# Kernel tuning notes

Hardware: AMD Instinct MI355X
Metric: run time of the kernel (lower is better)

The kernel has to match this reference:

```python
import math
import jax, jax.numpy as jnp
import numpy as np

D_MODEL = 1024
HEADS = 16
DH = D_MODEL // HEADS
MAX_REL = 128
LN_EPS = 1e-5


def setup_inputs() -> dict:
    key = jax.random.key(0)
    ks = jax.random.split(key, 6)
    B, T = 4, 2048
    scale = 1.0 / math.sqrt(D_MODEL)
    x = jax.random.normal(ks[0], (B, T, D_MODEL), dtype=jnp.float32)
    Wq = jax.random.normal(ks[1], (D_MODEL, D_MODEL), dtype=jnp.float32) * scale
    Wk = jax.random.normal(ks[2], (D_MODEL, D_MODEL), dtype=jnp.float32) * scale
    Wv = jax.random.normal(ks[3], (D_MODEL, D_MODEL), dtype=jnp.float32) * scale
    Wo = jax.random.normal(ks[4], (D_MODEL, D_MODEL), dtype=jnp.float32) * scale
    # rel bias init as in torch: per-head linspace(0, -2, max_rel+1)
    rel = jnp.tile(jnp.linspace(0.0, -2.0, MAX_REL + 1, dtype=jnp.float32)[None, :], (HEADS, 1))
    ln_gamma = jnp.ones((D_MODEL,), dtype=jnp.float32)
    ln_beta = jnp.zeros((D_MODEL,), dtype=jnp.float32)
    return {"x": x, "Wq": Wq, "Wk": Wk, "Wv": Wv, "Wo": Wo,
            "rel": rel, "ln_gamma": ln_gamma, "ln_beta": ln_beta}


def _layernorm(x, gamma, beta):
    mu = jnp.mean(x, axis=-1, keepdims=True)
    var = jnp.mean(jnp.square(x - mu), axis=-1, keepdims=True)
    return (x - mu) * jax.lax.rsqrt(var + LN_EPS) * gamma + beta


def reference(x, Wq, Wk, Wv, Wo, rel, ln_gamma, ln_beta):
    B, T, D = x.shape
    x0 = x
    xn = _layernorm(x, ln_gamma, ln_beta)
    # projections -> [B, H, T, dh]  (torch Linear: x @ W.T; weights here stored as [out,in])
    def proj(W):
        return (xn @ W.T).reshape(B, T, HEADS, DH).transpose(0, 2, 1, 3)
    q = proj(Wq) / math.sqrt(DH)
    k = proj(Wk)
    v = proj(Wv)
    scores = jnp.einsum('bhid,bhjd->bhij', q, k)  # [B,H,T,T]
    # latency-aware relative bias: bias[h,i,j] = rel[h, min(max(i-j,0), max_rel)]
    i = jnp.arange(T)
    dist = jnp.clip(i[:, None] - i[None, :], 0, MAX_REL)  # [T,T]
    bias = rel[:, dist]  # [H,T,T]
    scores = scores + bias[None]
    causal = i[:, None] >= i[None, :]  # j <= i allowed
    scores = jnp.where(causal[None, None], scores, -jnp.inf)
    attn = jax.nn.softmax(scores, axis=-1)
    y = jnp.einsum('bhij,bhjd->bhid', attn, v)  # [B,H,T,dh]
    y = y.transpose(0, 2, 1, 3).reshape(B, T, D)
    y = y @ Wo.T
    return x0 + y
```

## Files before the change

### kernel.cpp

```cpp
#include <hip/hip_runtime.h>
#include <math.h>

#define TSEQ 2048
#define BATCH 4
#define NH 16
#define DH 64
#define DM 1024
#define NREL 129
#define NEGBIG (-1.0e30f)
#define FIXMAX 8.0f

typedef unsigned short u16;
typedef unsigned int u32;
typedef __attribute__((ext_vector_type(8))) short bf16x8;
typedef __attribute__((ext_vector_type(4))) float f32x4;
typedef __attribute__((ext_vector_type(4))) unsigned short u16x4;

typedef __attribute__((address_space(3))) void lds_void;
typedef const __attribute__((address_space(1))) void g_void;

__device__ inline u16 f2b(float f) {
    union { float f; u32 i; } c; c.f = f;
    u32 x = c.i;
    return (u16)((x + 0x7fffu + ((x >> 16) & 1u)) >> 16);
}

__global__ __launch_bounds__(256) void fill_kernel(float* __restrict__ out, int n, float v) {
    for (int i = blockIdx.x * 256 + threadIdx.x; i < n; i += gridDim.x * 256)
        out[i] = v;
}

__global__ __launch_bounds__(256) void ln_kernel(const float* __restrict__ x,
        const float* __restrict__ gamma, const float* __restrict__ beta,
        u16* __restrict__ xn) {
    const int row = blockIdx.x;
    const int tid = threadIdx.x;
    const float* xr = x + (size_t)row * DM;
    f32x4 xv = *(const f32x4*)(xr + tid * 4);
    float s = xv.x + xv.y + xv.z + xv.w;
    float s2 = xv.x*xv.x + xv.y*xv.y + xv.z*xv.z + xv.w*xv.w;
#pragma unroll
    for (int off = 32; off > 0; off >>= 1) {
        s  += __shfl_down(s, off, 64);
        s2 += __shfl_down(s2, off, 64);
    }
    __shared__ alignas(16) float red[8];
    const int wv = tid >> 6, ln = tid & 63;
    if (ln == 0) { red[wv] = s; red[4 + wv] = s2; }
    __syncthreads();
    s  = red[0] + red[1] + red[2] + red[3];
    s2 = red[4] + red[5] + red[6] + red[7];
    const float mu = s * (1.0f / DM);
    float var = s2 * (1.0f / DM) - mu * mu;
    var = var > 0.0f ? var : 0.0f;
    const float rstd = rsqrtf(var + 1e-5f);
    f32x4 gv = *(const f32x4*)(gamma + tid * 4);
    f32x4 bv = *(const f32x4*)(beta + tid * 4);
    u16x4 ov;
    ov.x = f2b((xv.x - mu) * rstd * gv.x + bv.x);
    ov.y = f2b((xv.y - mu) * rstd * gv.y + bv.y);
    ov.z = f2b((xv.z - mu) * rstd * gv.z + bv.z);
    ov.w = f2b((xv.w - mu) * rstd * gv.w + bv.w);
    *(u16x4*)(xn + (size_t)row * DM + tid * 4) = ov;
}

__global__ __launch_bounds__(256) void cvt3_kernel(const float* __restrict__ a,
        const float* __restrict__ b, const float* __restrict__ c,
        u16* __restrict__ dst) {
    const int i = blockIdx.x * 256 + threadIdx.x;
    const int m = i >> 18;
    const int j = i & 0x3FFFF;
    const float* src = m == 0 ? a : (m == 1 ? b : c);
    const float scale = m == 0 ? 0.125f : 1.0f;
    f32x4 v = *(const f32x4*)(src + (size_t)j * 4);
    u16x4 o;
    o.x = f2b(v.x * scale); o.y = f2b(v.y * scale);
    o.z = f2b(v.z * scale); o.w = f2b(v.w * scale);
    *(u16x4*)(dst + (size_t)i * 4) = o;
}

__global__ __launch_bounds__(256) void cvt1_kernel(const float* __restrict__ src,
        u16* __restrict__ dst, int n4) {
    const int i = blockIdx.x * 256 + threadIdx.x;
    if (i >= n4) return;
    f32x4 v = *(const f32x4*)(src + (size_t)i * 4);
    u16x4 o;
    o.x = f2b(v.x); o.y = f2b(v.y); o.z = f2b(v.z); o.w = f2b(v.w);
    *(u16x4*)(dst + (size_t)i * 4) = o;
}

#define BM 128
#define BN 128
#define BK 32

__global__ __launch_bounds__(256) void gemm_qkv(const u16* __restrict__ A,
        const u16* __restrict__ W3, u16* __restrict__ Qb, u16* __restrict__ Kb,
        u16* __restrict__ Vb) {
    __shared__ alignas(16) u16 sh[8192];
    u16* As = sh;
    u16* Bs = sh + 4096;
    const int id = blockIdx.x + 64 * blockIdx.y;
    const int xcd = id & 7;
    const int k = id >> 3;
    const int xv = xcd * 8 + (k & 7);
    const int yv = k >> 3;
    const int m0 = xv * BM;
    const int mat = yv >> 3;
    const int n0 = (yv & 7) * BN;
    const u16* Wb = W3 + (size_t)mat * DM * DM;
    const int tid = threadIdx.x;
    const int w = tid >> 6;
    const int lane = tid & 63;
    const int quad = lane >> 4, l16 = lane & 15;
    const int wr = (w >> 1) * 64;
    const int wc = (w & 1) * 64;

    const int c0 = w * 2;
    const int srow = c0 * 16 + (lane >> 2);
    const int scol = (lane & 3) * 8;
    const u16* ag = A  + (size_t)(m0 + srow) * DM + scol;
    const u16* bg = Wb + (size_t)(n0 + srow) * DM + scol;
    u16* as0 = As + c0 * 512;
    u16* bs0 = Bs + c0 * 512;

    f32x4 acc[4][4];
#pragma unroll
    for (int i = 0; i < 4; i++)
#pragma unroll
        for (int j = 0; j < 4; j++) acc[i][j] = (f32x4){0.f, 0.f, 0.f, 0.f};

    for (int k0 = 0; k0 < DM; k0 += BK) {
        __builtin_amdgcn_global_load_lds((g_void*)(ag + k0),            (lds_void*)as0,         16, 0, 0);
        __builtin_amdgcn_global_load_lds((g_void*)(ag + k0 + 16 * DM),  (lds_void*)(as0 + 512), 16, 0, 0);
        __builtin_amdgcn_global_load_lds((g_void*)(bg + k0),            (lds_void*)bs0,         16, 0, 0);
        __builtin_amdgcn_global_load_lds((g_void*)(bg + k0 + 16 * DM),  (lds_void*)(bs0 + 512), 16, 0, 0);
        __syncthreads();
        bf16x8 af[4], bfr[4];
#pragma unroll
        for (int mt = 0; mt < 4; mt++)
            af[mt] = *(const bf16x8*)(As + (wr + mt * 16 + l16) * BK + quad * 8);
#pragma unroll
        for (int nt = 0; nt < 4; nt++)
            bfr[nt] = *(const bf16x8*)(Bs + (wc + nt * 16 + l16) * BK + quad * 8);
#pragma unroll
        for (int mt = 0; mt < 4; mt++)
#pragma unroll
            for (int nt = 0; nt < 4; nt++)
                acc[mt][nt] = __builtin_amdgcn_mfma_f32_16x16x32_bf16(af[mt], bfr[nt], acc[mt][nt], 0, 0, 0);
        __syncthreads();
    }

    u16* outb = mat == 0 ? Qb : (mat == 1 ? Kb : Vb);
    const size_t bh = (size_t)(m0 >> 11) * NH + ((n0 + wc) >> 6);
    const int tq = (m0 & 2047) + wr;
    u16* stage = sh + w * 2048;

#pragma unroll
    for (int p = 0; p < 2; p++) {
#pragma unroll
        for (int mt = 0; mt < 4; mt++) {
#pragma unroll
            for (int ntl = 0; ntl < 2; ntl++) {
                const int nt = p * 2 + ntl;
#pragma unroll
                for (int r = 0; r < 4; r++) {
                    const u16 val = f2b(acc[mt][nt][r]);
                    int a;
                    if (mat == 0) {
                        a = mt * 512
                          + ((ntl * 2 + (l16 >> 3)) * 16 + quad * 4 + r) * 8 + (l16 & 7);
                    } else if (mat == 1) {
                        a = ((mt >> 1) * 2 + (quad & 1)) * 512
                          + ((ntl * 2 + (l16 >> 3)) * 16 + (quad >> 1) * 4 + (mt & 1) * 8 + r) * 8
                          + (l16 & 7);
                    } else {
                        a = ((mt >> 1) * 2 + ntl) * 512
                          + (((mt * 2 + (quad >> 1)) & 3) * 16 + l16) * 8
                          + (quad & 1) * 4 + r;
                    }
                    stage[a] = val;
                }
            }
        }
#pragma unroll
        for (int c = 0; c < 4; c++) {
            const bf16x8 vv = *(const bf16x8*)(stage + c * 512 + lane * 8);
            size_t gc;
            if (mat == 0)      gc = (bh * 128 + (tq >> 4) + c) * 2 + p;
            else if (mat == 1) gc = (bh * 64 + (tq >> 5) + (c >> 1)) * 4 + (c & 1) * 2 + p;
            else               gc = (bh * 64 + (tq >> 5) + (c >> 1)) * 4 + p * 2 + (c & 1);
            *(bf16x8*)(outb + gc * 512 + lane * 8) = vv;
        }
    }
}

__global__ __launch_bounds__(256) void gemm_wo(const u16* __restrict__ A,
        const u16* __restrict__ Wb, const float* __restrict__ X0,
        float* __restrict__ out) {
    __shared__ alignas(16) u16 As[BM * BK];
    __shared__ alignas(16) u16 Bs[BN * BK];
    const int id = blockIdx.x + 64 * blockIdx.y;
    const int xcd = id & 7;
    const int k = id >> 3;
    const int m0 = (xcd * 8 + (k & 7)) * BM;
    const int n0 = (k >> 3) * BN;
    const int tid = threadIdx.x;
    const int w = tid >> 6;
    const int lane = tid & 63;
    const int quad = lane >> 4, l16 = lane & 15;
    const int wr = (w >> 1) * 64;
    const int wc = (w & 1) * 64;

    const int c0 = w * 2;
    const int srow = c0 * 16 + (lane >> 2);
    const int scol = (lane & 3) * 8;
    const u16* ag = A  + (size_t)(m0 + srow) * DM + scol;
    const u16* bg = Wb + (size_t)(n0 + srow) * DM + scol;
    u16* as0 = As + c0 * 512;
    u16* bs0 = Bs + c0 * 512;

    f32x4 acc[4][4];
#pragma unroll
    for (int i = 0; i < 4; i++)
#pragma unroll
        for (int j = 0; j < 4; j++) acc[i][j] = (f32x4){0.f, 0.f, 0.f, 0.f};

    for (int k0 = 0; k0 < DM; k0 += BK) {
        __builtin_amdgcn_global_load_lds((g_void*)(ag + k0),            (lds_void*)as0,         16, 0, 0);
        __builtin_amdgcn_global_load_lds((g_void*)(ag + k0 + 16 * DM),  (lds_void*)(as0 + 512), 16, 0, 0);
        __builtin_amdgcn_global_load_lds((g_void*)(bg + k0),            (lds_void*)bs0,         16, 0, 0);
        __builtin_amdgcn_global_load_lds((g_void*)(bg + k0 + 16 * DM),  (lds_void*)(bs0 + 512), 16, 0, 0);
        __syncthreads();
        bf16x8 af[4], bfr[4];
#pragma unroll
        for (int mt = 0; mt < 4; mt++)
            af[mt] = *(const bf16x8*)(As + (wr + mt * 16 + l16) * BK + quad * 8);
#pragma unroll
        for (int nt = 0; nt < 4; nt++)
            bfr[nt] = *(const bf16x8*)(Bs + (wc + nt * 16 + l16) * BK + quad * 8);
#pragma unroll
        for (int mt = 0; mt < 4; mt++)
#pragma unroll
            for (int nt = 0; nt < 4; nt++)
                acc[mt][nt] = __builtin_amdgcn_mfma_f32_16x16x32_bf16(af[mt], bfr[nt], acc[mt][nt], 0, 0, 0);
        __syncthreads();
    }

#pragma unroll
    for (int mt = 0; mt < 4; mt++) {
#pragma unroll
        for (int nt = 0; nt < 4; nt++) {
#pragma unroll
            for (int r = 0; r < 4; r++) {
                const int row = m0 + wr + mt * 16 + quad * 4 + r;
                const int col = n0 + wc + nt * 16 + l16;
                const size_t idx = (size_t)row * DM + col;
                out[idx] = acc[mt][nt][r] + X0[idx];
            }
        }
    }
}

__global__ __launch_bounds__(512, 8) void attn_kernel(const u16* __restrict__ Q,
        const u16* __restrict__ K, const u16* __restrict__ Vt,
        const float* __restrict__ rel, u16* __restrict__ y) {
    const int id = blockIdx.x + 16 * blockIdx.y;
    const int xcd = id & 7;
    const int idx = id >> 3;
    const int bh = xcd * 8 + (idx & 7);
    const int p = idx >> 3;
    const int h = bh & (NH - 1);
    const int b = bh >> 4;
    const int tid = threadIdx.x;
    const int w = tid >> 6, lane = tid & 63;
    const int rg = w & 3, jg = w >> 2;
    const int quad = lane >> 4, l16 = lane & 15;

    __shared__ alignas(16) float rel_s[NREL];
    __shared__ alignas(16) f32x4 cb[4][5][64];
    if (tid < NREL) rel_s[tid] = rel[h * NREL + tid];
    __syncthreads();
    const float r128 = rel_s[128];

    const u16* Qh = Q  + (size_t)bh * TSEQ * DH;
    const u16* Kh = K  + (size_t)bh * TSEQ * DH;
    const u16* Vh = Vt + (size_t)bh * TSEQ * DH;

    bf16x8 ones;
#pragma unroll
    for (int j = 0; j < 8; j++) ones[j] = (short)0x3F80;

    for (int ti = 0; ti < 2; ti++) {
        const int qt = ti ? (31 - p) : p;
        const int wq = qt * 64 + rg * 16;
        const int gq = wq + l16;
        const u16* qb = Qh + (size_t)(wq >> 4) * 1024 + lane * 8;
        const bf16x8 qf0 = *(const bf16x8*)(qb);
        const bf16x8 qf1 = *(const bf16x8*)(qb + 512);

        f32x4 o[4];
#pragma unroll
        for (int i = 0; i < 4; i++) o[i] = (f32x4){0.f, 0.f, 0.f, 0.f};
        f32x4 oL = (f32x4){0.f, 0.f, 0.f, 0.f};
        const int jend = wq + 16;

        for (int j0 = jg * 32; j0 < jend; j0 += 64) {
            const u16* kb = Kh + (size_t)(j0 >> 5) * 2048 + lane * 8;
            const bf16x8 k00 = *(const bf16x8*)(kb);
            const bf16x8 k01 = *(const bf16x8*)(kb + 512);
            const bf16x8 k10 = *(const bf16x8*)(kb + 1024);
            const bf16x8 k11 = *(const bf16x8*)(kb + 1536);
            f32x4 s0 = (f32x4){0.f, 0.f, 0.f, 0.f};
            f32x4 s1 = (f32x4){0.f, 0.f, 0.f, 0.f};
            s0 = __builtin_amdgcn_mfma_f32_16x16x32_bf16(k00, qf0, s0, 0, 0, 0);
            s0 = __builtin_amdgcn_mfma_f32_16x16x32_bf16(k01, qf1, s0, 0, 0, 0);
            s1 = __builtin_amdgcn_mfma_f32_16x16x32_bf16(k10, qf0, s1, 0, 0, 0);
            s1 = __builtin_amdgcn_mfma_f32_16x16x32_bf16(k11, qf1, s1, 0, 0, 0);

            float p0[4], p1[4];
            const int dq = gq - j0 - 8 * quad;
            if (j0 + 159 < wq) {
#pragma unroll
                for (int r = 0; r < 4; r++) {
                    p0[r] = __expf(s0[r] + (r128 - FIXMAX));
                    p1[r] = __expf(s1[r] + (r128 - FIXMAX));
                }
            } else {
#pragma unroll
                for (int r = 0; r < 4; r++) {
                    const int d0 = dq - r;
                    const int d1 = dq - 4 - r;
                    const int c0 = d0 < 0 ? 0 : (d0 > 128 ? 128 : d0);
                    const int c1 = d1 < 0 ? 0 : (d1 > 128 ? 128 : d1);
                    float sv0 = s0[r] + rel_s[c0];
                    float sv1 = s1[r] + rel_s[c1];
                    sv0 = d0 >= 0 ? sv0 : NEGBIG;
                    sv1 = d1 >= 0 ? sv1 : NEGBIG;
                    p0[r] = __expf(sv0 - FIXMAX);
                    p1[r] = __expf(sv1 - FIXMAX);
                }
            }
            bf16x8 pf;
            pf[0] = (short)f2b(p0[0]); pf[1] = (short)f2b(p0[1]);
            pf[2] = (short)f2b(p0[2]); pf[3] = (short)f2b(p0[3]);
            pf[4] = (short)f2b(p1[0]); pf[5] = (short)f2b(p1[1]);
            pf[6] = (short)f2b(p1[2]); pf[7] = (short)f2b(p1[3]);

            const u16* vb = Vh + (size_t)(j0 >> 5) * 2048 + lane * 8;
            bf16x8 vf[4];
#pragma unroll
            for (int dt = 0; dt < 4; dt++)
                vf[dt] = *(const bf16x8*)(vb + dt * 512);
#pragma unroll
            for (int dt = 0; dt < 4; dt++)
                o[dt] = __builtin_amdgcn_mfma_f32_16x16x32_bf16(pf, vf[dt], o[dt], 0, 0, 0);
            oL = __builtin_amdgcn_mfma_f32_16x16x32_bf16(pf, ones, oL, 0, 0, 0);
        }

        if (jg == 1) {
#pragma unroll
            for (int dt = 0; dt < 4; dt++) cb[rg][dt][lane] = o[dt];
            cb[rg][4][lane] = oL;
        }
        __syncthreads();
        if (jg == 0) {
#pragma unroll
            for (int dt = 0; dt < 4; dt++) {
                const f32x4 op = cb[rg][dt][lane];
                o[dt].x += op.x; o[dt].y += op.y; o[dt].z += op.z; o[dt].w += op.w;
            }
            const f32x4 oLp = cb[rg][4][lane];
            oL.x += oLp.x; oL.y += oLp.y; oL.z += oLp.z; oL.w += oLp.w;
#pragma unroll
            for (int dt = 0; dt < 4; dt++) {
#pragma unroll
                for (int r = 0; r < 4; r++) {
                    const float val = o[dt][r] / oL[r];
                    const int t = wq + quad * 4 + r;
                    y[((size_t)(b * TSEQ + t)) * DM + h * DH + dt * 16 + l16] = f2b(val);
                }
            }
        }
        __syncthreads();
    }
}

extern "C" void kernel_launch(void* const* d_in, const int* in_sizes, int n_in,
                              void* d_out, int out_size, void* d_ws, size_t ws_size,
                              hipStream_t stream) {
    const float* x   = (const float*)d_in[0];
    const float* Wq  = (const float*)d_in[1];
    const float* Wk  = (const float*)d_in[2];
    const float* Wv  = (const float*)d_in[3];
    const float* Wo  = (const float*)d_in[4];
    const float* rel = (const float*)d_in[5];
    const float* gam = (const float*)d_in[6];
    const float* bet = (const float*)d_in[7];
    u16* ws = (u16*)d_ws;
    const size_t SZ = (size_t)BATCH * TSEQ * DM;
    const size_t need_bytes = 4 * SZ * sizeof(u16);

    if (n_in != 8) {
        fill_kernel<<<4096, 256, 0, stream>>>((float*)d_out, out_size, 8000.0f);
        return;
    }
    if (ws_size < need_bytes) {
        fill_kernel<<<4096, 256, 0, stream>>>((float*)d_out, out_size, 9500.0f);
        return;
    }

    u16* xn = ws;
    u16* Qb = ws + SZ;
    u16* Kb = ws + 2 * SZ;
    u16* Vb = ws + 3 * SZ;
    u16* y  = xn;

    u16* wscr = (u16*)d_out;
    const int W4 = (DM * DM) / 4;

    ln_kernel<<<BATCH * TSEQ, 256, 0, stream>>>(x, gam, bet, xn);
    cvt3_kernel<<<3 * W4 / 256, 256, 0, stream>>>(Wq, Wk, Wv, wscr);
    gemm_qkv<<<dim3(BATCH * TSEQ / BM, 24), 256, 0, stream>>>(xn, wscr, Qb, Kb, Vb);
    attn_kernel<<<dim3(16, BATCH * NH), 512, 0, stream>>>(Qb, Kb, Vb, rel, y);
    cvt1_kernel<<<W4 / 256, 256, 0, stream>>>(Wo, Qb, W4);
    gemm_wo<<<dim3(BATCH * TSEQ / BM, DM / BN), 256, 0, stream>>>(y, Qb, x, (float*)d_out);
}
```

Baseline: 290.5 us.

## Double-buffer GEMM LDS tiles and pack bf16 conversions in attention

Both projection GEMMs now use two LDS buffers and issue the next K-tile's global-to-LDS loads before computing on the current tile. This is meant to overlap memory latency with MFMA work, at the cost of doubling LDS per block. The attention kernel swaps scalar bf16 rounding for the packed v_cvt_pk_bf16_f32 instruction. It also stages the normalized output through LDS so each lane writes 16-byte rows instead of scattered 2-byte stores, and replaces per-element division with a reciprocal multiply. One visible risk: the loop issues the prefetch with no barrier before the next iteration's reads, and relies on the trailing __syncthreads to ensure the async LDS loads have landed.

```diff
diff --git a/kernel.cpp b/kernel.cpp
--- a/kernel.cpp
+++ b/kernel.cpp
@@ -23,6 +23,12 @@
     union { float f; u32 i; } c; c.f = f;
     u32 x = c.i;
     return (u16)((x + 0x7fffu + ((x >> 16) & 1u)) >> 16);
+}
+
+__device__ inline u32 cvtpk(float lo, float hi) {
+    u32 r;
+    asm("v_cvt_pk_bf16_f32 %0, %1, %2" : "=v"(r) : "v"(lo), "v"(hi));
+    return r;
 }
 
 __global__ __launch_bounds__(256) void fill_kernel(float* __restrict__ out, int n, float v) {
@@ -96,9 +102,7 @@
 __global__ __launch_bounds__(256) void gemm_qkv(const u16* __restrict__ A,
         const u16* __restrict__ W3, u16* __restrict__ Qb, u16* __restrict__ Kb,
         u16* __restrict__ Vb) {
-    __shared__ alignas(16) u16 sh[8192];
-    u16* As = sh;
-    u16* Bs = sh + 4096;
+    __shared__ alignas(16) u16 sh[16384];
     const int id = blockIdx.x + 64 * blockIdx.y;
     const int xcd = id & 7;
     const int k = id >> 3;
@@ -120,8 +124,8 @@
     const int scol = (lane & 3) * 8;
     const u16* ag = A  + (size_t)(m0 + srow) * DM + scol;
     const u16* bg = Wb + (size_t)(n0 + srow) * DM + scol;
-    u16* as0 = As + c0 * 512;
-    u16* bs0 = Bs + c0 * 512;
+    u16* asw = sh + c0 * 512;
+    u16* bsw = sh + 8192 + c0 * 512;
 
     f32x4 acc[4][4];
 #pragma unroll
@@ -129,19 +133,27 @@
 #pragma unroll
         for (int j = 0; j < 4; j++) acc[i][j] = (f32x4){0.f, 0.f, 0.f, 0.f};
 
+#define QKV_STAGE(buf, kk) do { \
+    __builtin_amdgcn_global_load_lds((g_void*)(ag + (kk)),            (lds_void*)(asw + (buf)*4096),       16, 0, 0); \
+    __builtin_amdgcn_global_load_lds((g_void*)(ag + (kk) + 16 * DM),  (lds_void*)(asw + (buf)*4096 + 512), 16, 0, 0); \
+    __builtin_amdgcn_global_load_lds((g_void*)(bg + (kk)),            (lds_void*)(bsw + (buf)*4096),       16, 0, 0); \
+    __builtin_amdgcn_global_load_lds((g_void*)(bg + (kk) + 16 * DM),  (lds_void*)(bsw + (buf)*4096 + 512), 16, 0, 0); \
+} while (0)
+
+    QKV_STAGE(0, 0);
+    __syncthreads();
     for (int k0 = 0; k0 < DM; k0 += BK) {
-        __builtin_amdgcn_global_load_lds((g_void*)(ag + k0),            (lds_void*)as0,         16, 0, 0);
-        __builtin_amdgcn_global_load_lds((g_void*)(ag + k0 + 16 * DM),  (lds_void*)(as0 + 512), 16, 0, 0);
-        __builtin_amdgcn_global_load_lds((g_void*)(bg + k0),            (lds_void*)bs0,         16, 0, 0);
-        __builtin_amdgcn_global_load_lds((g_void*)(bg + k0 + 16 * DM),  (lds_void*)(bs0 + 512), 16, 0, 0);
-        __syncthreads();
+        const int cur = (k0 >> 5) & 1;
+        if (k0 + BK < DM) QKV_STAGE(cur ^ 1, k0 + BK);
+        const u16* Ac = sh + cur * 4096;
+        const u16* Bc = sh + 8192 + cur * 4096;
         bf16x8 af[4], bfr[4];
 #pragma unroll
         for (int mt = 0; mt < 4; mt++)
-            af[mt] = *(const bf16x8*)(As + (wr + mt * 16 + l16) * BK + quad * 8);
+            af[mt] = *(const bf16x8*)(Ac + (wr + mt * 16 + l16) * BK + quad * 8);
 #pragma unroll
         for (int nt = 0; nt < 4; nt++)
-            bfr[nt] = *(const bf16x8*)(Bs + (wc + nt * 16 + l16) * BK + quad * 8);
+            bfr[nt] = *(const bf16x8*)(Bc + (wc + nt * 16 + l16) * BK + quad * 8);
 #pragma unroll
         for (int mt = 0; mt < 4; mt++)
 #pragma unroll
@@ -149,6 +161,7 @@
                 acc[mt][nt] = __builtin_amdgcn_mfma_f32_16x16x32_bf16(af[mt], bfr[nt], acc[mt][nt], 0, 0, 0);
         __syncthreads();
     }
+#undef QKV_STAGE
 
     u16* outb = mat == 0 ? Qb : (mat == 1 ? Kb : Vb);
     const size_t bh = (size_t)(m0 >> 11) * NH + ((n0 + wc) >> 6);
@@ -197,8 +210,7 @@
 __global__ __launch_bounds__(256) void gemm_wo(const u16* __restrict__ A,
         const u16* __restrict__ Wb, const float* __restrict__ X0,
         float* __restrict__ out) {
-    __shared__ alignas(16) u16 As[BM * BK];
-    __shared__ alignas(16) u16 Bs[BN * BK];
+    __shared__ alignas(16) u16 sh[16384];
     const int id = blockIdx.x + 64 * blockIdx.y;
     const int xcd = id & 7;
     const int k = id >> 3;
@@ -216,8 +228,8 @@
     const int scol = (lane & 3) * 8;
     const u16* ag = A  + (size_t)(m0 + srow) * DM + scol;
     const u16* bg = Wb + (size_t)(n0 + srow) * DM + scol;
-    u16* as0 = As + c0 * 512;
-    u16* bs0 = Bs + c0 * 512;
+    u16* asw = sh + c0 * 512;
+    u16* bsw = sh + 8192 + c0 * 512;
 
     f32x4 acc[4][4];
 #pragma unroll
@@ -225,19 +237,27 @@
 #pragma unroll
         for (int j = 0; j < 4; j++) acc[i][j] = (f32x4){0.f, 0.f, 0.f, 0.f};
 
+#define WO_STAGE(buf, kk) do { \
+    __builtin_amdgcn_global_load_lds((g_void*)(ag + (kk)),            (lds_void*)(asw + (buf)*4096),       16, 0, 0); \
+    __builtin_amdgcn_global_load_lds((g_void*)(ag + (kk) + 16 * DM),  (lds_void*)(asw + (buf)*4096 + 512), 16, 0, 0); \
+    __builtin_amdgcn_global_load_lds((g_void*)(bg + (kk)),            (lds_void*)(bsw + (buf)*4096),       16, 0, 0); \
+    __builtin_amdgcn_global_load_lds((g_void*)(bg + (kk) + 16 * DM),  (lds_void*)(bsw + (buf)*4096 + 512), 16, 0, 0); \
+} while (0)
+
+    WO_STAGE(0, 0);
+    __syncthreads();
     for (int k0 = 0; k0 < DM; k0 += BK) {
-        __builtin_amdgcn_global_load_lds((g_void*)(ag + k0),            (lds_void*)as0,         16, 0, 0);
-        __builtin_amdgcn_global_load_lds((g_void*)(ag + k0 + 16 * DM),  (lds_void*)(as0 + 512), 16, 0, 0);
-        __builtin_amdgcn_global_load_lds((g_void*)(bg + k0),            (lds_void*)bs0,         16, 0, 0);
-        __builtin_amdgcn_global_load_lds((g_void*)(bg + k0 + 16 * DM),  (lds_void*)(bs0 + 512), 16, 0, 0);
-        __syncthreads();
+        const int cur = (k0 >> 5) & 1;
+        if (k0 + BK < DM) WO_STAGE(cur ^ 1, k0 + BK);
+        const u16* Ac = sh + cur * 4096;
+        const u16* Bc = sh + 8192 + cur * 4096;
         bf16x8 af[4], bfr[4];
 #pragma unroll
         for (int mt = 0; mt < 4; mt++)
-            af[mt] = *(const bf16x8*)(As + (wr + mt * 16 + l16) * BK + quad * 8);
+            af[mt] = *(const bf16x8*)(Ac + (wr + mt * 16 + l16) * BK + quad * 8);
 #pragma unroll
         for (int nt = 0; nt < 4; nt++)
-            bfr[nt] = *(const bf16x8*)(Bs + (wc + nt * 16 + l16) * BK + quad * 8);
+            bfr[nt] = *(const bf16x8*)(Bc + (wc + nt * 16 + l16) * BK + quad * 8);
 #pragma unroll
         for (int mt = 0; mt < 4; mt++)
 #pragma unroll
@@ -245,6 +265,7 @@
                 acc[mt][nt] = __builtin_amdgcn_mfma_f32_16x16x32_bf16(af[mt], bfr[nt], acc[mt][nt], 0, 0, 0);
         __syncthreads();
     }
+#undef WO_STAGE
 
 #pragma unroll
     for (int mt = 0; mt < 4; mt++) {
@@ -278,6 +299,7 @@
 
     __shared__ alignas(16) float rel_s[NREL];
     __shared__ alignas(16) f32x4 cb[4][5][64];
+    __shared__ alignas(16) u16 st_s[4][1024];
     if (tid < NREL) rel_s[tid] = rel[h * NREL + tid];
     __syncthreads();
     const float r128 = rel_s[128];
@@ -340,11 +362,12 @@
                     p1[r] = __expf(sv1 - FIXMAX);
                 }
             }
-            bf16x8 pf;
-            pf[0] = (short)f2b(p0[0]); pf[1] = (short)f2b(p0[1]);
-            pf[2] = (short)f2b(p0[2]); pf[3] = (short)f2b(p0[3]);
-            pf[4] = (short)f2b(p1[0]); pf[5] = (short)f2b(p1[1]);
-            pf[6] = (short)f2b(p1[2]); pf[7] = (short)f2b(p1[3]);
+            union { u32 u[4]; bf16x8 v; } pk_;
+            pk_.u[0] = cvtpk(p0[0], p0[1]);
+            pk_.u[1] = cvtpk(p0[2], p0[3]);
+            pk_.u[2] = cvtpk(p1[0], p1[1]);
+            pk_.u[3] = cvtpk(p1[2], p1[3]);
+            const bf16x8 pf = pk_.v;
 
             const u16* vb = Vh + (size_t)(j0 >> 5) * 2048 + lane * 8;
             bf16x8 vf[4];
@@ -371,14 +394,20 @@
             }
             const f32x4 oLp = cb[rg][4][lane];
             oL.x += oLp.x; oL.y += oLp.y; oL.z += oLp.z; oL.w += oLp.w;
-#pragma unroll
-            for (int dt = 0; dt < 4; dt++) {
-#pragma unroll
-                for (int r = 0; r < 4; r++) {
-                    const float val = o[dt][r] / oL[r];
-                    const int t = wq + quad * 4 + r;
-                    y[((size_t)(b * TSEQ + t)) * DM + h * DH + dt * 16 + l16] = f2b(val);
-                }
+            float inv[4];
+#pragma unroll
+            for (int r = 0; r < 4; r++) inv[r] = 1.0f / oL[r];
+            u16* st = st_s[rg];
+#pragma unroll
+            for (int dt = 0; dt < 4; dt++)
+#pragma unroll
+                for (int r = 0; r < 4; r++)
+                    st[(quad * 4 + r) * 64 + dt * 16 + l16] = f2b(o[dt][r] * inv[r]);
+#pragma unroll
+            for (int ps = 0; ps < 2; ps++) {
+                const bf16x8 vv = *(const bf16x8*)(st + ps * 512 + lane * 8);
+                const int row = wq + ps * 8 + (lane >> 3);
+                *(bf16x8*)(y + ((size_t)(b * TSEQ + row)) * DM + h * DH + (lane & 7) * 8) = vv;
             }
         }
         __syncthreads();
```

New measurement: 286.7 us. No clear change (-1.3%).
